# Kernel optimization log

Hardware: AMD Instinct MI355X
Metric: run time of the kernel (lower is better)

Reference implementation:

```python
import jax, jax.numpy as jnp
import numpy as np

B_, L_, D_ = 2, 1024, 512   # batch, seq_len, dim
H_ = 8                      # num_heads, head_dim = 64
Q_ = 64                     # chunk size for the chunked semi-separable scan


def setup_inputs() -> dict:
    key = jax.random.key(0)
    ks = jax.random.split(key, 7)
    s = 1.0 / np.sqrt(D_)   # torch nn.Linear default init bound
    x = jax.random.normal(ks[0], (B_, L_, D_), dtype=jnp.float32)
    W_A = jax.random.uniform(ks[1], (D_, D_), jnp.float32, -s, s)
    b_A = jax.random.uniform(ks[2], (D_,), jnp.float32, -s, s)
    W_B = jax.random.uniform(ks[3], (D_, D_), jnp.float32, -s, s)
    b_B = jax.random.uniform(ks[4], (D_,), jnp.float32, -s, s)
    W_C = jax.random.uniform(ks[5], (D_, D_), jnp.float32, -s, s)
    b_C = jax.random.uniform(ks[6], (D_,), jnp.float32, -s, s)
    return {"x": x, "W_A": W_A, "b_A": b_A, "W_B": W_B, "b_B": b_B,
            "W_C": W_C, "b_C": b_C}


def _semi_separable_T(x, W_A, b_A, W_B, b_B, W_C, b_C):
    """T_ij = sum_d C_{i,d} * (prod_{k=j+1}^{i-1} A_{k,d}) * B_{j,d}, j <= i.

    Computed in log space with Mamba2-style chunking: all exponent
    differences are <= 0, so exp() underflows to 0 (the true limit)
    instead of producing inf/nan as a naive cumprod-quotient would.
    """
    B, L, D = x.shape
    H = H_
    Dh = D // H
    Q = Q_
    nc = L // Q
    NEG = -jnp.inf

    A = jax.nn.sigmoid(x @ W_A.T + b_A)    # [B,L,D], values in (0,1)
    Bf = x @ W_B.T + b_B
    C = x @ W_C.T + b_C

    def heads(t):
        return t.reshape(B, L, H, Dh).transpose(0, 2, 1, 3)  # [B,H,L,Dh]

    A, Bf, C = heads(A), heads(Bf), heads(C)

    S = jnp.cumsum(jnp.log(A), axis=2)                       # S[k] = sum_{0..k} log A
    Sm1 = jnp.concatenate([jnp.zeros_like(S[:, :, :1]), S[:, :, :-1]], axis=2)
    # prod_{k=j+1}^{i-1} A_k = exp(Sm1[i] - S[j])  for i >= j+1 (==1 at i=j+1)

    def chunk(t):
        return t.reshape(B, H, nc, Q, Dh)

    Sc, Sm1c, Bc, Cc = chunk(S), chunk(Sm1), chunk(Bf), chunk(C)

    qi = jnp.arange(Q)[:, None]
    ki = jnp.arange(Q)[None, :]
    lower = (qi > ki)[None, None, None, :, :, None]
    diag = (qi == ki)[None, None, None, :, :, None]

    # ---- diagonal blocks (within-chunk, strictly lower + diagonal) ----
    diff = Sm1c[:, :, :, :, None, :] - Sc[:, :, :, None, :, :]  # [B,H,nc,Q,Q,Dh], <=0 where q>k
    dec = jnp.where(lower, diff, jnp.where(diag, 0.0, NEG))     # q==k -> prod=1
    Tdiag = jnp.einsum('bhmqd,bhmqkd,bhmkd->bhmqk', Cc, jnp.exp(dec), Bc)

    # ---- cross blocks (chunk m queries vs chunk n<m keys) ----
    E = Sc[:, :, :, -1, :]                                      # S at last index of each chunk
    Eprev = jnp.concatenate([jnp.zeros_like(E[:, :, :1]), E[:, :, :-1]], axis=2)
    qf = Cc * jnp.exp(Sm1c - Eprev[:, :, :, None, :])           # exponent <= 0
    kf = Bc * jnp.exp(E[:, :, :, None, :] - Sc)                 # exponent <= 0
    mi = jnp.arange(nc)[:, None]
    ni = jnp.arange(nc)[None, :]
    cross_mask = (ni < mi)[None, None, :, :, None]
    Dcross = jnp.exp(jnp.where(cross_mask,
                               Eprev[:, :, :, None, :] - E[:, :, None, :, :],
                               NEG))                            # [B,H,nc,nc,Dh]
    T = jnp.einsum('bhmqd,bhmnd,bhnkd->bhmqnk', qf, Dcross, kf)

    idx = jnp.arange(nc)
    T = T.at[:, :, idx, :, idx, :].set(jnp.moveaxis(Tdiag, 2, 0))
    return T.reshape(B, H, L, L)


def reference(x, W_A, b_A, W_B, b_B, W_C, b_C):
    return _semi_separable_T(x, W_A, b_A, W_B, b_B, W_C, b_C)
```

## Files before the change

kernel.cpp:

```cpp
#include <hip/hip_runtime.h>
#include <math.h>

#define BB 2
#define LL 1024
#define DD 512
#define HH 8
#define DHD 64
#define QQ 64
#define NCC 16

typedef __attribute__((ext_vector_type(8))) short s8b;
typedef __attribute__((ext_vector_type(4))) float f4;

__device__ __forceinline__ void gld16(const void* g, void* l) {
    __builtin_amdgcn_global_load_lds(
        (const __attribute__((address_space(1))) unsigned int*)g,
        (__attribute__((address_space(3))) unsigned int*)l, 16, 0, 0);
}

__device__ __forceinline__ void bf16split(float f, unsigned short& h, unsigned short& l) {
    unsigned u  = __float_as_uint(f);
    unsigned hb = (u + 0x7FFFu + ((u >> 16) & 1u)) & 0xFFFF0000u;
    float fh = __uint_as_float(hb);
    float fl = f - fh;
    unsigned ul = __float_as_uint(fl);
    unsigned lb = (ul + 0x7FFFu + ((ul >> 16) & 1u)) >> 16;
    h = (unsigned short)(hb >> 16);
    l = (unsigned short)lb;
}

__device__ __forceinline__ unsigned pk2(unsigned short a, unsigned short b) {
    return (unsigned)a | ((unsigned)b << 16);
}

__global__ __launch_bounds__(256) void convert_split(
    const float* __restrict__ x, const float* __restrict__ Wa,
    const float* __restrict__ Wb, const float* __restrict__ Wc,
    unsigned short* __restrict__ xh, unsigned short* __restrict__ xl,
    unsigned short* __restrict__ wh, unsigned short* __restrict__ wl)
{
    const int g = blockIdx.x * 256 + threadIdx.x;
    const float* src;
    unsigned short *dh, *dl;
    if (g < 262144) {
        const size_t off = (size_t)g * 4;
        src = x + off; dh = xh + off; dl = xl + off;
    } else {
        const size_t j = (size_t)(g - 262144) * 4;
        const int wsel = (int)(j >> 18);
        const size_t r = j & 262143;
        src = (wsel == 0 ? Wa : (wsel == 1 ? Wb : Wc)) + r;
        dh = wh + j; dl = wl + j;
    }
    const float4 v = *(const float4*)src;
    const float f[4] = {v.x, v.y, v.z, v.w};
    unsigned short h[4], l[4];
    #pragma unroll
    for (int i = 0; i < 4; ++i) bf16split(f[i], h[i], l[i]);
    *(uint2*)dh = make_uint2(pk2(h[0], h[1]), pk2(h[2], h[3]));
    *(uint2*)dl = make_uint2(pk2(l[0], l[1]), pk2(l[2], l[3]));
}

__global__ __launch_bounds__(512) void gemm3_fused(
    const unsigned short* __restrict__ xh, const unsigned short* __restrict__ xl,
    const unsigned short* __restrict__ wh, const unsigned short* __restrict__ wl,
    const float* __restrict__ ba, const float* __restrict__ bb, const float* __restrict__ bc,
    float* __restrict__ logA, float* __restrict__ Bf, float* __restrict__ Cf,
    float* __restrict__ csum)
{
    __shared__ unsigned char lds[65536];
    __shared__ float csv[64];

    const int bm = blockIdx.x >> 3;
    const int bn = blockIdx.x & 7;
    const int m0 = bm << 6, o0 = bn << 6;
    const int t = threadIdx.x, wv = t >> 6, ln = t & 63;
    const int l15 = ln & 15, l4 = ln >> 4;
    const int wr = (wv >> 2) << 5;
    const int wc = (wv & 3) << 4;

    const unsigned short* hp = (wv < 2) ? xh : wh + (size_t)((wv - 2) >> 1) * 262144;
    const unsigned short* lp = (wv < 2) ? xl : wl + (size_t)((wv - 2) >> 1) * 262144;
    const unsigned short* sp2 = ((wv & 1) ? lp : hp) + (size_t)((wv < 2) ? m0 : o0) * DD;
    const int abase = wv * 4096;

    const int rl = ln >> 2;
    const int sl = ln & 3;
    size_t gofs[4];
    #pragma unroll
    for (int s = 0; s < 4; ++s) {
        const int rowg = s * 16 + rl;
        const int kfc  = sl ^ ((rowg >> 1) & 3);
        gofs[s] = (size_t)rowg * DD + kfc * 8;
    }

    f4 acc[3][2] = {};

    auto STAGE = [&](int buf, int kt) {
        unsigned char* base = lds + buf * 32768 + abase;
        #pragma unroll
        for (int s = 0; s < 4; ++s)
            gld16(sp2 + kt + gofs[s], base + s * 1024);
    };

    auto ldso = [&](int row, int kg) {
        return row * 64 + ((kg ^ ((row >> 1) & 3)) << 4);
    };

    auto COMPUTE = [&](int buf) {
        const unsigned char* base = lds + buf * 32768;
        const s8b ah0 = *(const s8b*)(base + 0*4096 + ldso(wr      + l15, l4));
        const s8b ah1 = *(const s8b*)(base + 0*4096 + ldso(wr + 16 + l15, l4));
        const s8b al0 = *(const s8b*)(base + 1*4096 + ldso(wr      + l15, l4));
        const s8b al1 = *(const s8b*)(base + 1*4096 + ldso(wr + 16 + l15, l4));
        #pragma unroll
        for (int s = 0; s < 3; ++s) {
            const s8b bh = *(const s8b*)(base + (2 + 2*s)*4096 + ldso(wc + l15, l4));
            const s8b bl = *(const s8b*)(base + (3 + 2*s)*4096 + ldso(wc + l15, l4));
            acc[s][0] = __builtin_amdgcn_mfma_f32_16x16x32_bf16(ah0, bh, acc[s][0], 0, 0, 0);
            acc[s][1] = __builtin_amdgcn_mfma_f32_16x16x32_bf16(ah1, bh, acc[s][1], 0, 0, 0);
            acc[s][0] = __builtin_amdgcn_mfma_f32_16x16x32_bf16(ah0, bl, acc[s][0], 0, 0, 0);
            acc[s][1] = __builtin_amdgcn_mfma_f32_16x16x32_bf16(ah1, bl, acc[s][1], 0, 0, 0);
            acc[s][0] = __builtin_amdgcn_mfma_f32_16x16x32_bf16(al0, bh, acc[s][0], 0, 0, 0);
            acc[s][1] = __builtin_amdgcn_mfma_f32_16x16x32_bf16(al1, bh, acc[s][1], 0, 0, 0);
        }
    };

    STAGE(0, 0);
    __syncthreads();
    int cur = 0;
    for (int it = 0; it < 16; ++it) {
        if (it < 15) STAGE(cur ^ 1, (it + 1) * 32);
        COMPUTE(cur);
        __syncthreads();
        cur ^= 1;
    }

    const int col = o0 + wc + l15;
    const float bva = ba[col], bvb = bb[col], bvc = bc[col];
    float asum = 0.f;
    #pragma unroll
    for (int ms = 0; ms < 2; ++ms) {
        const int row0 = m0 + wr + ms * 16 + l4 * 4;
        #pragma unroll
        for (int r = 0; r < 4; ++r) {
            const size_t o = (size_t)(row0 + r) * DD + col;
            float va = acc[0][ms][r] + bva;
            va = fminf(va, 0.f) - log1pf(__expf(-fabsf(va)));
            logA[o] = va;
            asum += va;
            Bf[o] = acc[1][ms][r] + bvb;
            Cf[o] = acc[2][ms][r] + bvc;
        }
    }

    asum += __shfl_xor(asum, 16);
    asum += __shfl_xor(asum, 32);
    if (wv < 4 && l4 == 0) csv[wc + l15] = asum;
    __syncthreads();
    if (wv >= 4 && l4 == 0) {
        const int blkc = (((bm >> 4) * 8 + bn) << 4) + (bm & 15);
        csum[(size_t)blkc * DHD + wc + l15] = csv[wc + l15] + asum;
    }
}

__global__ __launch_bounds__(256) void scan_diag(
    const float* __restrict__ logA, const float* __restrict__ Bf,
    const float* __restrict__ Cf, const float* __restrict__ csum,
    float* __restrict__ qf, float* __restrict__ kf,
    float* __restrict__ coff, float* __restrict__ out)
{
    __shared__ float part[4][DHD];
    __shared__ float smA[DHD][65];
    __shared__ float smB[DHD][65];
    __shared__ float smC[DHD][65];

    const int blk = blockIdx.x;
    const int bh = blk >> 4, c = blk & 15;
    const int b = bh >> 3, h = bh & 7;
    const int t = threadIdx.x;
    const int d = t & 63, w = t >> 6;

    const size_t gbase = (size_t)(b * LL + c * QQ + w * 16) * DD + h * DHD + d;
    float lar[16];
    float ps = 0.f;
    #pragma unroll
    for (int i = 0; i < 16; ++i) {
        lar[i] = logA[gbase + (size_t)i * DD];
        ps += lar[i];
    }
    part[w][d] = ps;
    __syncthreads();

    const size_t cs0 = ((size_t)bh << 4) * DHD + d;
    float off = 0.f;
    for (int cc = 0; cc < c; ++cc) off += csum[cs0 + (size_t)cc * DHD];
    const float tot = part[0][d] + part[1][d] + part[2][d] + part[3][d];
    if (t < DHD) {
        coff[((size_t)bh * 17 + c) * DHD + t] = off;
        if (c == NCC - 1) coff[((size_t)bh * 17 + 16) * DHD + t] = off + tot;
    }

    float run = 0.f;
    for (int ww = 0; ww < 4; ++ww) if (ww < w) run += part[ww][d];

    const size_t hbase = ((size_t)bh * LL + c * QQ + w * 16) * DHD + d;
    #pragma unroll
    for (int i = 0; i < 16; ++i) {
        const size_t gi = gbase + (size_t)i * DD;
        const float cv = Cf[gi];
        const float bv = Bf[gi];
        qf[hbase + (size_t)i * DHD] = cv * __expf(run);
        run += lar[i];
        const int rloc = w * 16 + i;
        smC[d][rloc] = run;
        smA[d][rloc] = cv;
        smB[d][rloc] = bv;
        kf[hbase + (size_t)i * DHD] = bv * __expf(tot - run);
    }
    __syncthreads();

    const int q0 = ((t >> 4) & 15) << 2;
    const int k0 = (t & 15) << 2;

    float acc[4][4] = {};
    if (q0 + 3 >= k0) {
        #pragma unroll 2
        for (int dd = 0; dd < DHD; ++dd) {
            const float4 cq = *(const float4*)&smA[dd][q0];
            const float4 bk = *(const float4*)&smB[dd][k0];
            const float4 sk = *(const float4*)&smC[dd][k0];
            const float cqa[4] = {cq.x, cq.y, cq.z, cq.w};
            const float bka[4] = {bk.x, bk.y, bk.z, bk.w};
            const float ska[4] = {sk.x, sk.y, sk.z, sk.w};
            float s1a[4];
            #pragma unroll
            for (int i = 0; i < 4; ++i) {
                const int qi = q0 + i;
                s1a[i] = (qi == 0) ? 0.f : smC[dd][qi - 1];
            }
            #pragma unroll
            for (int i = 0; i < 4; ++i) {
                #pragma unroll
                for (int j = 0; j < 4; ++j) {
                    const int qi = q0 + i, kj = k0 + j;
                    const float wgt = (qi > kj) ? __expf(s1a[i] - ska[j])
                                                : ((qi == kj) ? 1.f : 0.f);
                    acc[i][j] += cqa[i] * wgt * bka[j];
                }
            }
        }
    }
    const size_t outrow0 = ((size_t)bh * LL + (size_t)c * QQ) * LL + (size_t)c * QQ;
    #pragma unroll
    for (int i = 0; i < 4; ++i)
        *(float4*)&out[outrow0 + (size_t)(q0 + i) * LL + k0] =
            make_float4(acc[i][0], acc[i][1], acc[i][2], acc[i][3]);
}

__global__ __launch_bounds__(256) void band_row(
    const float* __restrict__ qf, const float* __restrict__ kf,
    const float* __restrict__ coff, float* __restrict__ out)
{
    __shared__ unsigned char lds[49152];
    unsigned char* const l_qh = lds;
    unsigned char* const l_ql = lds + 8192;

    const int half = blockIdx.x & 1;
    const int m    = (blockIdx.x >> 1) & 15;
    const int bh   = blockIdx.x >> 5;
    const int n0   = half << 3;

    const int t  = threadIdx.x;
    const int wv = t >> 6;
    const int ln = t & 63;
    const int l15 = ln & 15;
    const int l4  = ln >> 4;
    const int wr = (wv >> 1) << 5;
    const int wc = (wv & 1) << 5;

    const int srow = t >> 2;
    const int skc  = (t & 3) << 4;
    const int slot0 = skc >> 3;

    const size_t cb = (size_t)bh * 17 * DHD;
    const size_t outbase = ((size_t)bh * LL + (size_t)m * QQ) * LL;

    for (int n = (m >= n0 ? m + 1 : n0); n < n0 + 8; ++n) {
        const size_t ob = outbase + (size_t)srow * LL + (size_t)n * QQ + skc;
        const float4 z = make_float4(0.f, 0.f, 0.f, 0.f);
        *(float4*)&out[ob + 0]  = z;
        *(float4*)&out[ob + 4]  = z;
        *(float4*)&out[ob + 8]  = z;
        *(float4*)&out[ob + 12] = z;
    }

    const int ne = (m < n0 + 8) ? m : (n0 + 8);
    if (n0 >= ne) return;

    float cm[16];
    #pragma unroll
    for (int g = 0; g < 4; ++g) {
        const float4 a = *(const float4*)&coff[cb + (size_t)m * DHD + skc + g * 4];
        cm[g*4+0]=a.x; cm[g*4+1]=a.y; cm[g*4+2]=a.z; cm[g*4+3]=a.w;
    }

    {
        const size_t qb = ((size_t)bh * LL + (size_t)m * QQ + srow) * DHD + skc;
        float v[16];
        #pragma unroll
        for (int g = 0; g < 4; ++g) {
            const float4 x4 = *(const float4*)&qf[qb + g * 4];
            v[g*4+0]=x4.x; v[g*4+1]=x4.y; v[g*4+2]=x4.z; v[g*4+3]=x4.w;
        }
        unsigned short h[16], l[16];
        #pragma unroll
        for (int i = 0; i < 16; ++i) bf16split(v[i], h[i], l[i]);
        *(uint4*)(l_qh + slot0*1024 + srow*16) =
            make_uint4(pk2(h[0],h[1]), pk2(h[2],h[3]), pk2(h[4],h[5]), pk2(h[6],h[7]));
        *(uint4*)(l_qh + (slot0+1)*1024 + srow*16) =
            make_uint4(pk2(h[8],h[9]), pk2(h[10],h[11]), pk2(h[12],h[13]), pk2(h[14],h[15]));
        *(uint4*)(l_ql + slot0*1024 + srow*16) =
            make_uint4(pk2(l[0],l[1]), pk2(l[2],l[3]), pk2(l[4],l[5]), pk2(l[6],l[7]));
        *(uint4*)(l_ql + (slot0+1)*1024 + srow*16) =
            make_uint4(pk2(l[8],l[9]), pk2(l[10],l[11]), pk2(l[12],l[13]), pk2(l[14],l[15]));
    }

    auto STAGE_K = [&](int buf, int n) {
        unsigned char* const kh_b = lds + 16384 + buf * 16384;
        unsigned char* const kl_b = kh_b + 8192;
        float dv[16];
        #pragma unroll
        for (int g = 0; g < 4; ++g) {
            const float4 c4 = *(const float4*)&coff[cb + (size_t)(n + 1) * DHD + skc + g * 4];
            dv[g*4+0] = __expf(cm[g*4+0] - c4.x);
            dv[g*4+1] = __expf(cm[g*4+1] - c4.y);
            dv[g*4+2] = __expf(cm[g*4+2] - c4.z);
            dv[g*4+3] = __expf(cm[g*4+3] - c4.w);
        }
        const size_t kb = ((size_t)bh * LL + (size_t)n * QQ + srow) * DHD + skc;
        float v[16];
        #pragma unroll
        for (int g = 0; g < 4; ++g) {
            const float4 x4 = *(const float4*)&kf[kb + g * 4];
            v[g*4+0]=x4.x*dv[g*4+0]; v[g*4+1]=x4.y*dv[g*4+1];
            v[g*4+2]=x4.z*dv[g*4+2]; v[g*4+3]=x4.w*dv[g*4+3];
        }
        unsigned short h[16], l[16];
        #pragma unroll
        for (int i = 0; i < 16; ++i) bf16split(v[i], h[i], l[i]);
        *(uint4*)(kh_b + slot0*1024 + srow*16) =
            make_uint4(pk2(h[0],h[1]), pk2(h[2],h[3]), pk2(h[4],h[5]), pk2(h[6],h[7]));
        *(uint4*)(kh_b + (slot0+1)*1024 + srow*16) =
            make_uint4(pk2(h[8],h[9]), pk2(h[10],h[11]), pk2(h[12],h[13]), pk2(h[14],h[15]));
        *(uint4*)(kl_b + slot0*1024 + srow*16) =
            make_uint4(pk2(l[0],l[1]), pk2(l[2],l[3]), pk2(l[4],l[5]), pk2(l[6],l[7]));
        *(uint4*)(kl_b + (slot0+1)*1024 + srow*16) =
            make_uint4(pk2(l[8],l[9]), pk2(l[10],l[11]), pk2(l[12],l[13]), pk2(l[14],l[15]));
    };

    STAGE_K(0, n0);
    __syncthreads();

    int cur = 0;
    for (int n = n0; n < ne; ++n) {
        if (n + 1 < ne) STAGE_K(cur ^ 1, n + 1);

        const unsigned char* const kh_b = lds + 16384 + cur * 16384;
        const unsigned char* const kl_b = kh_b + 8192;

        f4 acc[2][2] = {};
        #pragma unroll
        for (int ks = 0; ks < 2; ++ks) {
            const int ka = (ks * 4 + l4) * 1024;
            const s8b kh0 = *(const s8b*)(kh_b + ka + (wr      + l15) * 16);
            const s8b kh1 = *(const s8b*)(kh_b + ka + (wr + 16 + l15) * 16);
            const s8b kl0 = *(const s8b*)(kl_b + ka + (wr      + l15) * 16);
            const s8b kl1 = *(const s8b*)(kl_b + ka + (wr + 16 + l15) * 16);
            const s8b qh0 = *(const s8b*)(l_qh + ka + (wc      + l15) * 16);
            const s8b qh1 = *(const s8b*)(l_qh + ka + (wc + 16 + l15) * 16);
            const s8b ql0 = *(const s8b*)(l_ql + ka + (wc      + l15) * 16);
            const s8b ql1 = *(const s8b*)(l_ql + ka + (wc + 16 + l15) * 16);

            acc[0][0] = __builtin_amdgcn_mfma_f32_16x16x32_bf16(kh0, qh0, acc[0][0], 0, 0, 0);
            acc[0][1] = __builtin_amdgcn_mfma_f32_16x16x32_bf16(kh0, qh1, acc[0][1], 0, 0, 0);
            acc[1][0] = __builtin_amdgcn_mfma_f32_16x16x32_bf16(kh1, qh0, acc[1][0], 0, 0, 0);
            acc[1][1] = __builtin_amdgcn_mfma_f32_16x16x32_bf16(kh1, qh1, acc[1][1], 0, 0, 0);
            acc[0][0] = __builtin_amdgcn_mfma_f32_16x16x32_bf16(kh0, ql0, acc[0][0], 0, 0, 0);
            acc[0][1] = __builtin_amdgcn_mfma_f32_16x16x32_bf16(kh0, ql1, acc[0][1], 0, 0, 0);
            acc[1][0] = __builtin_amdgcn_mfma_f32_16x16x32_bf16(kh1, ql0, acc[1][0], 0, 0, 0);
            acc[1][1] = __builtin_amdgcn_mfma_f32_16x16x32_bf16(kh1, ql1, acc[1][1], 0, 0, 0);
            acc[0][0] = __builtin_amdgcn_mfma_f32_16x16x32_bf16(kl0, qh0, acc[0][0], 0, 0, 0);
            acc[0][1] = __builtin_amdgcn_mfma_f32_16x16x32_bf16(kl0, qh1, acc[0][1], 0, 0, 0);
            acc[1][0] = __builtin_amdgcn_mfma_f32_16x16x32_bf16(kl1, qh0, acc[1][0], 0, 0, 0);
            acc[1][1] = __builtin_amdgcn_mfma_f32_16x16x32_bf16(kl1, qh1, acc[1][1], 0, 0, 0);
        }

        #pragma unroll
        for (int ms = 0; ms < 2; ++ms) {
            #pragma unroll
            for (int ns = 0; ns < 2; ++ns) {
                const int q  = wc + ns * 16 + l15;
                const int k0 = wr + ms * 16 + l4 * 4;
                *(float4*)&out[outbase + (size_t)q * LL + (size_t)n * QQ + k0] =
                    make_float4(acc[ms][ns][0], acc[ms][ns][1], acc[ms][ns][2], acc[ms][ns][3]);
            }
        }
        __syncthreads();
        cur ^= 1;
    }
}

extern "C" void kernel_launch(void* const* d_in, const int* in_sizes, int n_in,
                              void* d_out, int out_size, void* d_ws, size_t ws_size,
                              hipStream_t stream) {
    const float* x  = (const float*)d_in[0];
    const float* Wa = (const float*)d_in[1];
    const float* ba = (const float*)d_in[2];
    const float* Wb = (const float*)d_in[3];
    const float* bb = (const float*)d_in[4];
    const float* Wc = (const float*)d_in[5];
    const float* bc = (const float*)d_in[6];
    float* out = (float*)d_out;
    float* ws  = (float*)d_ws;

    const size_t NBLD = (size_t)BB * LL * DD;
    float* logA = ws;
    float* Bf   = ws + 1 * NBLD;
    float* Cf   = ws + 2 * NBLD;
    float* qf   = ws + 4 * NBLD;
    float* kf   = ws + 5 * NBLD;
    float* coff = ws + 6 * NBLD;
    float* csum = coff + (size_t)BB * HH * 17 * DHD;

    unsigned short* xh  = (unsigned short*)(ws + 3 * NBLD);
    unsigned short* xl  = xh + 1048576;
    unsigned short* whp = xl + 1048576;
    unsigned short* wlp = whp + 786432;

    convert_split<<<1792, 256, 0, stream>>>(x, Wa, Wb, Wc, xh, xl, whp, wlp);
    gemm3_fused<<<256, 512, 0, stream>>>(xh, xl, whp, wlp, ba, bb, bc, logA, Bf, Cf, csum);
    scan_diag<<<BB * HH * NCC, 256, 0, stream>>>(logA, Bf, Cf, csum, qf, kf, coff, out);
    band_row<<<BB * HH * NCC * 2, 256, 0, stream>>>(qf, kf, coff, out);
}
```

Baseline: 81.78 us.

## Load K fragments directly into registers in band_row, dropping LDS double buffer

The band_row kernel no longer stages the scaled K chunk through a double-buffered LDS region. Each lane now loads its own K rows from global memory, applies the decay scaling, splits to bf16 hi/lo, and packs the MFMA operands in registers. This removes the per-iteration __syncthreads and cuts LDS from 48KB to 16KB, which should allow more resident blocks. The cost is redundant global loads and exp/split work, since the two waves sharing a row range each load and convert the same K data, and there is no prefetch overlap any more.

```diff
diff --git a/kernel.cpp b/kernel.cpp
--- a/kernel.cpp
+++ b/kernel.cpp
@@ -262,7 +262,7 @@
     const float* __restrict__ qf, const float* __restrict__ kf,
     const float* __restrict__ coff, float* __restrict__ out)
 {
-    __shared__ unsigned char lds[49152];
+    __shared__ unsigned char lds[16384];
     unsigned char* const l_qh = lds;
     unsigned char* const l_ql = lds + 8192;
 
@@ -297,13 +297,6 @@
 
     const int ne = (m < n0 + 8) ? m : (n0 + 8);
     if (n0 >= ne) return;
-
-    float cm[16];
-    #pragma unroll
-    for (int g = 0; g < 4; ++g) {
-        const float4 a = *(const float4*)&coff[cb + (size_t)m * DHD + skc + g * 4];
-        cm[g*4+0]=a.x; cm[g*4+1]=a.y; cm[g*4+2]=a.z; cm[g*4+3]=a.w;
-    }
 
     {
         const size_t qb = ((size_t)bh * LL + (size_t)m * QQ + srow) * DHD + skc;
@@ -325,58 +318,61 @@
         *(uint4*)(l_ql + (slot0+1)*1024 + srow*16) =
             make_uint4(pk2(l[8],l[9]), pk2(l[10],l[11]), pk2(l[12],l[13]), pk2(l[14],l[15]));
     }
-
-    auto STAGE_K = [&](int buf, int n) {
-        unsigned char* const kh_b = lds + 16384 + buf * 16384;
-        unsigned char* const kl_b = kh_b + 8192;
-        float dv[16];
-        #pragma unroll
-        for (int g = 0; g < 4; ++g) {
-            const float4 c4 = *(const float4*)&coff[cb + (size_t)(n + 1) * DHD + skc + g * 4];
-            dv[g*4+0] = __expf(cm[g*4+0] - c4.x);
-            dv[g*4+1] = __expf(cm[g*4+1] - c4.y);
-            dv[g*4+2] = __expf(cm[g*4+2] - c4.z);
-            dv[g*4+3] = __expf(cm[g*4+3] - c4.w);
-        }
-        const size_t kb = ((size_t)bh * LL + (size_t)n * QQ + srow) * DHD + skc;
-        float v[16];
-        #pragma unroll
-        for (int g = 0; g < 4; ++g) {
-            const float4 x4 = *(const float4*)&kf[kb + g * 4];
-            v[g*4+0]=x4.x*dv[g*4+0]; v[g*4+1]=x4.y*dv[g*4+1];
-            v[g*4+2]=x4.z*dv[g*4+2]; v[g*4+3]=x4.w*dv[g*4+3];
-        }
-        unsigned short h[16], l[16];
-        #pragma unroll
-        for (int i = 0; i < 16; ++i) bf16split(v[i], h[i], l[i]);
-        *(uint4*)(kh_b + slot0*1024 + srow*16) =
-            make_uint4(pk2(h[0],h[1]), pk2(h[2],h[3]), pk2(h[4],h[5]), pk2(h[6],h[7]));
-        *(uint4*)(kh_b + (slot0+1)*1024 + srow*16) =
-            make_uint4(pk2(h[8],h[9]), pk2(h[10],h[11]), pk2(h[12],h[13]), pk2(h[14],h[15]));
-        *(uint4*)(kl_b + slot0*1024 + srow*16) =
-            make_uint4(pk2(l[0],l[1]), pk2(l[2],l[3]), pk2(l[4],l[5]), pk2(l[6],l[7]));
-        *(uint4*)(kl_b + (slot0+1)*1024 + srow*16) =
-            make_uint4(pk2(l[8],l[9]), pk2(l[10],l[11]), pk2(l[12],l[13]), pk2(l[14],l[15]));
-    };
-
-    STAGE_K(0, n0);
     __syncthreads();
 
-    int cur = 0;
+    float cmv[16];
+    #pragma unroll
+    for (int ks = 0; ks < 2; ++ks) {
+        const size_t o = cb + (size_t)m * DHD + ks * 32 + l4 * 8;
+        const float4 a0 = *(const float4*)&coff[o + 0];
+        const float4 a1 = *(const float4*)&coff[o + 4];
+        cmv[ks*8+0]=a0.x; cmv[ks*8+1]=a0.y; cmv[ks*8+2]=a0.z; cmv[ks*8+3]=a0.w;
+        cmv[ks*8+4]=a1.x; cmv[ks*8+5]=a1.y; cmv[ks*8+6]=a1.z; cmv[ks*8+7]=a1.w;
+    }
+
+    const int rA0 = wr + l15;
+    const int rA1 = wr + 16 + l15;
+
     for (int n = n0; n < ne; ++n) {
-        if (n + 1 < ne) STAGE_K(cur ^ 1, n + 1);
-
-        const unsigned char* const kh_b = lds + 16384 + cur * 16384;
-        const unsigned char* const kl_b = kh_b + 8192;
+        const size_t kb0 = ((size_t)bh * LL + (size_t)n * QQ + rA0) * DHD;
+        const size_t kb1 = ((size_t)bh * LL + (size_t)n * QQ + rA1) * DHD;
+        const size_t co  = cb + (size_t)(n + 1) * DHD;
 
         f4 acc[2][2] = {};
         #pragma unroll
         for (int ks = 0; ks < 2; ++ks) {
+            const int kcs = ks * 32 + l4 * 8;
+            float dv[8];
+            {
+                const float4 c0 = *(const float4*)&coff[co + kcs + 0];
+                const float4 c1 = *(const float4*)&coff[co + kcs + 4];
+                dv[0]=__expf(cmv[ks*8+0]-c0.x); dv[1]=__expf(cmv[ks*8+1]-c0.y);
+                dv[2]=__expf(cmv[ks*8+2]-c0.z); dv[3]=__expf(cmv[ks*8+3]-c0.w);
+                dv[4]=__expf(cmv[ks*8+4]-c1.x); dv[5]=__expf(cmv[ks*8+5]-c1.y);
+                dv[6]=__expf(cmv[ks*8+6]-c1.z); dv[7]=__expf(cmv[ks*8+7]-c1.w);
+            }
+            float va[8], vb[8];
+            {
+                const float4 x0 = *(const float4*)&kf[kb0 + kcs + 0];
+                const float4 x1 = *(const float4*)&kf[kb0 + kcs + 4];
+                va[0]=x0.x*dv[0]; va[1]=x0.y*dv[1]; va[2]=x0.z*dv[2]; va[3]=x0.w*dv[3];
+                va[4]=x1.x*dv[4]; va[5]=x1.y*dv[5]; va[6]=x1.z*dv[6]; va[7]=x1.w*dv[7];
+                const float4 y0 = *(const float4*)&kf[kb1 + kcs + 0];
+                const float4 y1 = *(const float4*)&kf[kb1 + kcs + 4];
+                vb[0]=y0.x*dv[0]; vb[1]=y0.y*dv[1]; vb[2]=y0.z*dv[2]; vb[3]=y0.w*dv[3];
+                vb[4]=y1.x*dv[4]; vb[5]=y1.y*dv[5]; vb[6]=y1.z*dv[6]; vb[7]=y1.w*dv[7];
+            }
+            unsigned short ha[8], la[8], hb[8], lb[8];
+            #pragma unroll
+            for (int i = 0; i < 8; ++i) { bf16split(va[i], ha[i], la[i]); bf16split(vb[i], hb[i], lb[i]); }
+            s8b kh0, kl0, kh1, kl1;
+            #pragma unroll
+            for (int i = 0; i < 8; ++i) {
+                kh0[i] = (short)ha[i]; kl0[i] = (short)la[i];
+                kh1[i] = (short)hb[i]; kl1[i] = (short)lb[i];
+            }
+
             const int ka = (ks * 4 + l4) * 1024;
-            const s8b kh0 = *(const s8b*)(kh_b + ka + (wr      + l15) * 16);
-            const s8b kh1 = *(const s8b*)(kh_b + ka + (wr + 16 + l15) * 16);
-            const s8b kl0 = *(const s8b*)(kl_b + ka + (wr      + l15) * 16);
-            const s8b kl1 = *(const s8b*)(kl_b + ka + (wr + 16 + l15) * 16);
             const s8b qh0 = *(const s8b*)(l_qh + ka + (wc      + l15) * 16);
             const s8b qh1 = *(const s8b*)(l_qh + ka + (wc + 16 + l15) * 16);
             const s8b ql0 = *(const s8b*)(l_ql + ka + (wc      + l15) * 16);
@@ -406,8 +402,6 @@
                     make_float4(acc[ms][ns][0], acc[ms][ns][1], acc[ms][ns][2], acc[ms][ns][3]);
             }
         }
-        __syncthreads();
-        cur ^= 1;
     }
 }
 
```

After: 91.04 us. 11.3% more time.
